# Performance work log

Hardware: AMD Instinct MI355X
Metric: run time of the kernel (lower is better)

The kernel has to match this reference:

```python
import jax, jax.numpy as jnp
import numpy as np

NUM_HEADS = 6
EPS = 1e-6

def setup_inputs() -> dict:
    key = jax.random.key(0)
    k1, k2, k3, k4, k5 = jax.random.split(key, 5)
    B, N, C = 8, 1024, 384
    x = jax.random.normal(k1, (B, N, C), dtype=jnp.float32)
    # torch nn.Linear weights stored here as [in, out] for y = x @ W
    w_qkv = jax.random.normal(k2, (C, 3 * C), dtype=jnp.float32) * 0.02
    w_out = jax.random.normal(k3, (C, C), dtype=jnp.float32) * 0.02
    b_out = jax.random.normal(k4, (C,), dtype=jnp.float32) * 0.02
    # non-negative random-walk visitation mask (avg visits per node)
    mask = jax.random.uniform(k5, (N, N), dtype=jnp.float32)
    return {"x": x, "w_qkv": w_qkv, "w_out": w_out, "b_out": b_out, "mask": mask}

def reference(x, w_qkv, w_out, b_out, mask):
    B, N, C = x.shape
    H = NUM_HEADS
    D = C // H
    qkv = x @ w_qkv                                   # [B,N,3C]
    q, k, v = jnp.split(qkv, 3, axis=-1)
    # [B,N,C] -> [B,H,N,D]
    to_heads = lambda t: t.reshape(B, N, H, D).transpose(0, 2, 1, 3)
    q, k, v = to_heads(q), to_heads(k), to_heads(v)
    # feature map: relu(x) + eps
    q = jax.nn.relu(q) + EPS
    k = jax.nn.relu(k) + EPS
    # masked linear kernel: (Phi(Q) Phi(K)^T * mask)
    kernel = jnp.einsum("bhnd,bhmd->bhnm", q, k) * mask  # [B,H,N,N]
    z = 1.0 / (kernel.sum(axis=-1, keepdims=True) + EPS)  # row normalizer
    out = jnp.einsum("bhnm,bhmd->bhnd", kernel, v) * z    # [B,H,N,D]
    out = out.transpose(0, 2, 1, 3).reshape(B, N, C)
    return out @ w_out + b_out
```

## Files before the change

kernel.cpp:

```cpp
#include <hip/hip_runtime.h>
#include <hip/hip_bf16.h>
#include <hip/hip_fp16.h>
#include <stdint.h>

typedef __hip_bfloat16 bf16;
typedef __attribute__((ext_vector_type(8))) short short8;
typedef __attribute__((ext_vector_type(4))) float f32x4;
typedef __attribute__((ext_vector_type(16))) float f32x16;
typedef __attribute__((ext_vector_type(4))) int int4v;
typedef __attribute__((ext_vector_type(4))) unsigned short ushort4v;

#define MFMA16(A,B,C) __builtin_amdgcn_mfma_f32_16x16x32_bf16(A,B,C,0,0,0)
#define MFMA32(A,B,C) __builtin_amdgcn_mfma_f32_32x32x16_bf16(A,B,C,0,0,0)

#define FENCE() asm volatile("" ::: "memory")
#define SBAR()  do { FENCE(); __builtin_amdgcn_s_barrier(); FENCE(); } while (0)
#define WAITVN(N) asm volatile("s_waitcnt vmcnt(" #N ")" ::: "memory")

static __device__ __forceinline__ void g2lds16(const void* g, void* l) {
  __builtin_amdgcn_global_load_lds(
      (__attribute__((address_space(1))) void*)(g),
      (__attribute__((address_space(3))) void*)(l), 16, 0, 0);
}

static __device__ __forceinline__ int swz8(int row, int kc) {
  return row * 8 + (kc ^ (row & 7));
}

static __device__ __forceinline__ unsigned short f2bf_bits(float f) {
  bf16 t = __float2bfloat16(f); unsigned short u; __builtin_memcpy(&u, &t, 2); return u;
}
static __device__ __forceinline__ unsigned short f2h_bits(float f) {
  __half t = __float2half(f); unsigned short u; __builtin_memcpy(&u, &t, 2); return u;
}

template<bool HALFOUT>
static __device__ __forceinline__ void tileT(const float* __restrict__ in,
                                             unsigned short* __restrict__ out,
                                             int R, int C, int tr, int tc, int tid,
                                             float (*tls)[65]) {
  const int rr0 = tid >> 4, c4 = tid & 15;
  #pragma unroll
  for (int rr = 0; rr < 4; ++rr) {
    int r = rr0 + rr * 16;
    float4 v = *(const float4*)(in + (size_t)(tr * 64 + r) * C + tc * 64 + c4 * 4);
    tls[r][c4 * 4 + 0] = v.x; tls[r][c4 * 4 + 1] = v.y;
    tls[r][c4 * 4 + 2] = v.z; tls[r][c4 * 4 + 3] = v.w;
  }
  __syncthreads();
  #pragma unroll
  for (int rr = 0; rr < 4; ++rr) {
    int r2 = rr0 + rr * 16;
    ushort4v o;
    #pragma unroll
    for (int k = 0; k < 4; ++k) {
      float f = tls[c4 * 4 + k][r2];
      o[k] = HALFOUT ? f2h_bits(f) : f2bf_bits(f);
    }
    *(ushort4v*)(out + (size_t)(tc * 64 + r2) * R + tr * 64 + c4 * 4) = o;
  }
}

__global__ __launch_bounds__(256)
void k_prep(const float* __restrict__ x, bf16* __restrict__ xb,
            const float* __restrict__ wqkv, unsigned short* __restrict__ wqkvT,
            const float* __restrict__ wout, unsigned short* __restrict__ woutT,
            const float* __restrict__ mask, unsigned short* __restrict__ maskT) {
  __shared__ float tls[64][65];
  const int bid = blockIdx.x, tid = threadIdx.x;
  if (bid < 768) {
    #pragma unroll
    for (int j = 0; j < 4; ++j) {
      int i = bid * 1024 + j * 256 + tid;
      float4 v = ((const float4*)x)[i];
      bf16* po = xb + (size_t)i * 4;
      po[0] = __float2bfloat16(v.x); po[1] = __float2bfloat16(v.y);
      po[2] = __float2bfloat16(v.z); po[3] = __float2bfloat16(v.w);
    }
  } else if (bid < 876) {
    int tt = bid - 768; tileT<false>(wqkv, wqkvT, 384, 1152, tt / 18, tt % 18, tid, tls);
  } else if (bid < 912) {
    int tt = bid - 876; tileT<false>(wout, woutT, 384, 384, tt / 6, tt % 6, tid, tls);
  } else {
    int tt = bid - 912; tileT<true>(mask, maskT, 1024, 1024, tt / 16, tt % 16, tid, tls);
  }
}

__global__ __launch_bounds__(256, 3)
void k_gemm_qkv(const bf16* __restrict__ A, const bf16* __restrict__ BT,
                bf16* __restrict__ Cb, bf16* __restrict__ vT)
{
  __shared__ __align__(16) bf16 As[128 * 64];
  __shared__ __align__(16) bf16 Bs[96 * 64];
  const int tid = threadIdx.x;
  const int wave = tid >> 6, lane = tid & 63;
  const int lhi = lane >> 4, llo = lane & 15;
  const int wr = wave >> 1, wc = wave & 1;
  const int mBase = blockIdx.x * 128, nBase = blockIdx.y * 96;
  const int K = 384, N = 1152;

  f32x4 acc[4][3] = {};

  for (int kt = 0; kt < K; kt += 64) {
    __syncthreads();
    #pragma unroll
    for (int i = 0; i < 4; ++i) {
      int c = i * 256 + tid;
      int row = c >> 3;
      int kc = (c & 7) ^ (row & 7);
      g2lds16(A + (size_t)(mBase + row) * K + kt + kc * 8, As + (c & ~63) * 8);
    }
    #pragma unroll
    for (int i = 0; i < 3; ++i) {
      int c = i * 256 + tid;
      int row = c >> 3;
      int kc = (c & 7) ^ (row & 7);
      g2lds16(BT + (size_t)(nBase + row) * K + kt + kc * 8, Bs + (c & ~63) * 8);
    }
    __syncthreads();
    for (int kk = 0; kk < 2; ++kk) {
      const int kc = kk * 4 + lhi;
      short8 a[4], b[3];
      #pragma unroll
      for (int mi = 0; mi < 4; ++mi)
        a[mi] = *(const short8*)(As + swz8(wr * 64 + mi * 16 + llo, kc) * 8);
      #pragma unroll
      for (int ni = 0; ni < 3; ++ni)
        b[ni] = *(const short8*)(Bs + swz8(wc * 48 + ni * 16 + llo, kc) * 8);
      #pragma unroll
      for (int mi = 0; mi < 4; ++mi)
        #pragma unroll
        for (int ni = 0; ni < 3; ++ni)
          acc[mi][ni] = MFMA16(a[mi], b[ni], acc[mi][ni]);
    }
  }

  const bool isV = (nBase >= 768);
  #pragma unroll
  for (int mi = 0; mi < 4; ++mi)
    #pragma unroll
    for (int ni = 0; ni < 3; ++ni) {
      const int colbase = nBase + wc * 48 + ni * 16;
      if (!isV) {
        #pragma unroll
        for (int j = 0; j < 4; ++j) {
          int row = mBase + wr * 64 + mi * 16 + lhi * 4 + j;
          int col = colbase + llo;
          float v = fmaxf(acc[mi][ni][j], 0.f) + 1e-6f;
          Cb[(size_t)row * N + col] = __float2bfloat16(v);
        }
      } else {
        int col = colbase + llo;
        int dall = col - 768, hh = dall >> 6, dd = dall & 63;
        int rowg = mBase + wr * 64 + mi * 16 + lhi * 4;
        int bb = rowg >> 10, nloc = rowg & 1023;
        ushort4v pk;
        #pragma unroll
        for (int j = 0; j < 4; ++j) pk[j] = f2bf_bits(acc[mi][ni][j]);
        *(ushort4v*)((unsigned short*)vT + (((size_t)bb * 6 + hh) * 64 + dd) * 1024 + nloc) = pk;
      }
    }
}

__global__ __launch_bounds__(256, 3)
void k_attn(const bf16* __restrict__ qkv,
            const bf16* __restrict__ vT,
            const __half* __restrict__ maskT,
            bf16* __restrict__ out)
{
  __shared__ __align__(16) bf16 Ks[2][64 * 64];
  __shared__ __align__(16) bf16 Vs[2][64 * 64];
  __shared__ float Ored[2][32][65];
  __shared__ float zred[2][2][32];

  const int bid = blockIdx.x;
  const int bh = bid % 48, qt = bid / 48;
  const int b = bh / 6, h = bh - b * 6;
  const int tid = threadIdx.x, wave = tid >> 6, lane = tid & 63;
  const int lq = lane & 31, lh = lane >> 5;
  const int wq = wave & 1, wm = wave >> 1;
  const size_t row0 = (size_t)b * 1024;
  const int qglob = qt * 64 + wq * 32 + lq;

  auto stageKV = [&](int mt, int buf) {
    #pragma unroll
    for (int i = 0; i < 2; ++i) {
      int c = (wave * 2 + i) * 64 + lane;
      int row = c >> 3;
      int kc = (c & 7) ^ (row & 7);
      g2lds16(qkv + (row0 + mt * 64 + row) * 1152 + 384 + h * 64 + kc * 8,
              Ks[buf] + (c & ~63) * 8);
      g2lds16(vT + ((size_t)bh * 64 + row) * 1024 + mt * 64 + kc * 8,
              Vs[buf] + (c & ~63) * 8);
    }
  };

  short8 bq[4];
  {
    const bf16* qp = qkv + (row0 + qglob) * 1152 + h * 64 + lh * 8;
    #pragma unroll
    for (int ks = 0; ks < 4; ++ks) bq[ks] = *(const short8*)(qp + ks * 16);
  }
  stageKV(0, 0);

  f32x16 accO[2] = {};
  float zl = 0.f;

  #pragma unroll 1
  for (int mt = 0; mt < 16; ++mt) {
    const int cur = mt & 1;
    const bf16* Kc = Ks[cur];
    const bf16* Vc = Vs[cur];

    if (mt < 15) {
      stageKV(mt + 1, cur ^ 1);
      WAITVN(4);
    } else {
      WAITVN(0);
    }
    SBAR();

    __half mv[16];
    {
      const int mrow0 = mt * 64 + wm * 32 + 4 * lh;
      #pragma unroll
      for (int g = 0; g < 4; ++g)
        #pragma unroll
        for (int j = 0; j < 4; ++j)
          mv[g * 4 + j] = maskT[(size_t)(mrow0 + 8 * g + j) * 1024 + qglob];
    }

    f32x16 st = {};
    #pragma unroll
    for (int ks = 0; ks < 4; ++ks) {
      int row = wm * 32 + lq;
      int cc = (ks * 2 + lh) ^ (row & 7);
      short8 af = *(const short8*)(Kc + (row * 8 + cc) * 8);
      st = MFMA32(af, bq[ks], st);
    }

    float p[16];
    {
      float zp = 0.f;
      #pragma unroll
      for (int r = 0; r < 16; ++r) {
        p[r] = st[r] * __half2float(mv[r]);
        zp += p[r];
      }
      zl += zp;
    }
    int u[4][2];
    #pragma unroll
    for (int g = 0; g < 4; ++g)
      #pragma unroll
      for (int c = 0; c < 2; ++c)
        asm("v_cvt_pk_bf16_f32 %0, %1, %2"
            : "=v"(u[g][c]) : "v"(p[4 * g + 2 * c]), "v"(p[4 * g + 2 * c + 1]));

    short8 pa[2];
    #pragma unroll
    for (int ks = 0; ks < 2; ++ks) {
      int A0 = u[2 * ks][0], A0b = u[2 * ks][1];
      int A1 = u[2 * ks + 1][0], A1b = u[2 * ks + 1][1];
      int x0 = __shfl_xor(A0, 32), x1 = __shfl_xor(A0b, 32);
      int y0 = __shfl_xor(A1, 32), y1 = __shfl_xor(A1b, 32);
      int4v iv;
      iv.x = lh ? y0 : A0;
      iv.y = lh ? y1 : A0b;
      iv.z = lh ? A1 : x0;
      iv.w = lh ? A1b : x1;
      pa[ks] = *(short8*)&iv;
    }

    #pragma unroll
    for (int db = 0; db < 2; ++db)
      #pragma unroll
      for (int ks = 0; ks < 2; ++ks) {
        int row = db * 32 + lq;
        int cc = (wm * 4 + ks * 2 + lh) ^ (row & 7);
        short8 vb = *(const short8*)(Vc + (row * 8 + cc) * 8);
        accO[db] = MFMA32(pa[ks], vb, accO[db]);
      }

    asm volatile("s_waitcnt lgkmcnt(0)" ::: "memory");
    __builtin_amdgcn_sched_barrier(0);
    SBAR();
  }

  zl += __shfl_xor(zl, 32);
  zred[wq][wm][lq] = zl;
  if (wm == 1) {
    #pragma unroll
    for (int db = 0; db < 2; ++db)
      #pragma unroll
      for (int r = 0; r < 16; ++r) {
        int q = (r & 3) + 8 * (r >> 2) + 4 * lh;
        Ored[wq][q][db * 32 + lq] = accO[db][r];
      }
  }
  __syncthreads();
  if (wm == 0) {
    #pragma unroll
    for (int r = 0; r < 16; ++r) {
      int q = (r & 3) + 8 * (r >> 2) + 4 * lh;
      float zt = zred[wq][0][q] + zred[wq][1][q];
      float zi = 1.f / (zt + 1e-6f);
      int n = qt * 64 + wq * 32 + q;
      size_t orow = (row0 + n) * 384 + h * 64;
      #pragma unroll
      for (int db = 0; db < 2; ++db) {
        float val = (accO[db][r] + Ored[wq][q][db * 32 + lq]) * zi;
        out[orow + db * 32 + lq] = __float2bfloat16(val);
      }
    }
  }
}

__global__ __launch_bounds__(256, 3)
void k_gemm_out(const bf16* __restrict__ A, const bf16* __restrict__ BT,
                float* __restrict__ Cf, const float* __restrict__ bias)
{
  __shared__ __align__(16) bf16 As[64 * 64];
  __shared__ __align__(16) bf16 Bs[64 * 64];
  const int tid = threadIdx.x;
  const int wave = tid >> 6, lane = tid & 63;
  const int lq = lane & 31, lh = lane >> 5;
  const int wr = wave >> 1, wc = wave & 1;
  const int mBase = blockIdx.x * 64, nBase = blockIdx.y * 64;
  const int N = 384, K = 384;

  f32x16 acc = {};
  for (int kt = 0; kt < K; kt += 64) {
    __syncthreads();
    #pragma unroll
    for (int i = 0; i < 2; ++i) {
      int c = (wave * 2 + i) * 64 + lane;
      int row = c >> 3;
      int kc = (c & 7) ^ (row & 7);
      g2lds16(A  + (size_t)(mBase + row) * K + kt + kc * 8, As + (c & ~63) * 8);
      g2lds16(BT + (size_t)(nBase + row) * K + kt + kc * 8, Bs + (c & ~63) * 8);
    }
    __syncthreads();
    #pragma unroll
    for (int ks = 0; ks < 4; ++ks) {
      int ra = wr * 32 + lq, rb = wc * 32 + lq;
      short8 a = *(const short8*)(As + (ra * 8 + ((ks * 2 + lh) ^ (ra & 7))) * 8);
      short8 b = *(const short8*)(Bs + (rb * 8 + ((ks * 2 + lh) ^ (rb & 7))) * 8);
      acc = MFMA32(a, b, acc);
    }
  }
  #pragma unroll
  for (int r = 0; r < 16; ++r) {
    int row = mBase + wr * 32 + (r & 3) + 8 * (r >> 2) + 4 * lh;
    int col = nBase + wc * 32 + lq;
    Cf[(size_t)row * N + col] = acc[r] + bias[col];
  }
}

extern "C" void kernel_launch(void* const* d_in, const int* in_sizes, int n_in,
                              void* d_out, int out_size, void* d_ws, size_t ws_size,
                              hipStream_t stream) {
  (void)in_sizes; (void)n_in; (void)out_size; (void)ws_size;
  const float* x    = (const float*)d_in[0];
  const float* wqkv = (const float*)d_in[1];
  const float* wout = (const float*)d_in[2];
  const float* bout = (const float*)d_in[3];
  const float* mask = (const float*)d_in[4];
  float* outp = (float*)d_out;

  char* ws = (char*)d_ws;
  bf16*  xb    = (bf16*)(ws);
  bf16*  wqkvT = (bf16*)(ws + 6291456);
  bf16*  woutT = (bf16*)(ws + 7176192);
  bf16*  qkvb  = (bf16*)(ws + 7471104);
  bf16*  vTb   = (bf16*)(ws + 26345472);
  bf16*  ab    = (bf16*)(ws + 32636928);
  __half* maskT = (__half*)(ws + 38928384);

  k_prep<<<dim3(1168), dim3(256), 0, stream>>>(
      x, xb, wqkv, (unsigned short*)wqkvT, wout, (unsigned short*)woutT,
      mask, (unsigned short*)maskT);

  k_gemm_qkv<<<dim3(64, 12), dim3(256), 0, stream>>>(xb, wqkvT, qkvb, vTb);
  k_attn<<<dim3(768), dim3(256), 0, stream>>>(qkvb, vTb, maskT, ab);
  k_gemm_out<<<dim3(128, 6), dim3(256), 0, stream>>>(ab, woutT, outp, bout);
}
```

Before: 58.81 us.

## Triple-buffer K/V tiles, prefetch mask one tile ahead, drop second barrier

The attention kernel now keeps K/V tiles in a three-slot ring inside one shared buffer, which lets each iteration get by with a single barrier instead of two. The per-tile mask values are loaded one iteration early into alternating register arrays, so global mask latency overlaps with the current tile's MFMA work. The Ored/zred reduction scratch now aliases the K/V staging memory, so total LDS stays at about 48.5KB. In exchange, register pressure rises from the extra mask array, and the ring-buffer reuse depends on barrier ordering being correct.

```diff
diff --git a/kernel.cpp b/kernel.cpp
--- a/kernel.cpp
+++ b/kernel.cpp
@@ -168,10 +168,11 @@
             const __half* __restrict__ maskT,
             bf16* __restrict__ out)
 {
-  __shared__ __align__(16) bf16 Ks[2][64 * 64];
-  __shared__ __align__(16) bf16 Vs[2][64 * 64];
-  __shared__ float Ored[2][32][65];
-  __shared__ float zred[2][2][32];
+  __shared__ __align__(16) char smem[49664];
+  bf16* KsB = (bf16*)smem;
+  bf16* VsB = KsB + 3 * 4096;
+  float* OredF = (float*)smem;
+  float* zredF = (float*)(smem + 49152);
 
   const int bid = blockIdx.x;
   const int bh = bid % 48, qt = bid / 48;
@@ -189,10 +190,18 @@
       int row = c >> 3;
       int kc = (c & 7) ^ (row & 7);
       g2lds16(qkv + (row0 + mt * 64 + row) * 1152 + 384 + h * 64 + kc * 8,
-              Ks[buf] + (c & ~63) * 8);
+              KsB + buf * 4096 + (c & ~63) * 8);
       g2lds16(vT + ((size_t)bh * 64 + row) * 1024 + mt * 64 + kc * 8,
-              Vs[buf] + (c & ~63) * 8);
-    }
+              VsB + buf * 4096 + (c & ~63) * 8);
+    }
+  };
+  auto loadMask = [&](int mt, __half (&mv)[16]) {
+    const int mrow0 = mt * 64 + wm * 32 + 4 * lh;
+    #pragma unroll
+    for (int g = 0; g < 4; ++g)
+      #pragma unroll
+      for (int j = 0; j < 4; ++j)
+        mv[g * 4 + j] = maskT[(size_t)(mrow0 + 8 * g + j) * 1024 + qglob];
   };
 
   short8 bq[4];
@@ -201,34 +210,29 @@
     #pragma unroll
     for (int ks = 0; ks < 4; ++ks) bq[ks] = *(const short8*)(qp + ks * 16);
   }
-  stageKV(0, 0);
 
   f32x16 accO[2] = {};
   float zl = 0.f;
 
-  #pragma unroll 1
-  for (int mt = 0; mt < 16; ++mt) {
-    const int cur = mt & 1;
-    const bf16* Kc = Ks[cur];
-    const bf16* Vc = Vs[cur];
-
-    if (mt < 15) {
-      stageKV(mt + 1, cur ^ 1);
+  __half mvA[16], mvB[16];
+  stageKV(0, 0);
+  loadMask(0, mvA);
+
+  auto iter = [&](int t, __half (&mvUse)[16], __half (&mvPre)[16]) {
+    const int bc = t % 3;
+    const bf16* Kc = KsB + bc * 4096;
+    const bf16* Vc = VsB + bc * 4096;
+
+    if (t < 15) {
+      stageKV(t + 1, (t + 1) % 3);
       WAITVN(4);
     } else {
       WAITVN(0);
     }
+    asm volatile("s_waitcnt lgkmcnt(0)" ::: "memory");
     SBAR();
 
-    __half mv[16];
-    {
-      const int mrow0 = mt * 64 + wm * 32 + 4 * lh;
-      #pragma unroll
-      for (int g = 0; g < 4; ++g)
-        #pragma unroll
-        for (int j = 0; j < 4; ++j)
-          mv[g * 4 + j] = maskT[(size_t)(mrow0 + 8 * g + j) * 1024 + qglob];
-    }
+    if (t < 15) loadMask(t + 1, mvPre);
 
     f32x16 st = {};
     #pragma unroll
@@ -244,7 +248,7 @@
       float zp = 0.f;
       #pragma unroll
       for (int r = 0; r < 16; ++r) {
-        p[r] = st[r] * __half2float(mv[r]);
+        p[r] = st[r] * __half2float(mvUse[r]);
         zp += p[r];
       }
       zl += zp;
@@ -281,21 +285,24 @@
         short8 vb = *(const short8*)(Vc + (row * 8 + cc) * 8);
         accO[db] = MFMA32(pa[ks], vb, accO[db]);
       }
-
-    asm volatile("s_waitcnt lgkmcnt(0)" ::: "memory");
-    __builtin_amdgcn_sched_barrier(0);
-    SBAR();
-  }
+  };
+
+  #pragma unroll 1
+  for (int mt2 = 0; mt2 < 8; ++mt2) {
+    iter(2 * mt2,     mvA, mvB);
+    iter(2 * mt2 + 1, mvB, mvA);
+  }
+  __syncthreads();
 
   zl += __shfl_xor(zl, 32);
-  zred[wq][wm][lq] = zl;
+  zredF[(wq * 2 + wm) * 32 + lq] = zl;
   if (wm == 1) {
     #pragma unroll
     for (int db = 0; db < 2; ++db)
       #pragma unroll
       for (int r = 0; r < 16; ++r) {
         int q = (r & 3) + 8 * (r >> 2) + 4 * lh;
-        Ored[wq][q][db * 32 + lq] = accO[db][r];
+        OredF[(wq * 32 + q) * 65 + db * 32 + lq] = accO[db][r];
       }
   }
   __syncthreads();
@@ -303,13 +310,13 @@
     #pragma unroll
     for (int r = 0; r < 16; ++r) {
       int q = (r & 3) + 8 * (r >> 2) + 4 * lh;
-      float zt = zred[wq][0][q] + zred[wq][1][q];
+      float zt = zredF[wq * 2 * 32 + q] + zredF[(wq * 2 + 1) * 32 + q];
       float zi = 1.f / (zt + 1e-6f);
       int n = qt * 64 + wq * 32 + q;
       size_t orow = (row0 + n) * 384 + h * 64;
       #pragma unroll
       for (int db = 0; db < 2; ++db) {
-        float val = (accO[db][r] + Ored[wq][q][db * 32 + lq]) * zi;
+        float val = (accO[db][r] + OredF[(wq * 32 + q) * 65 + db * 32 + lq]) * zi;
         out[orow + db * 32 + lq] = __float2bfloat16(val);
       }
     }
```

Measured after the change: 57.03 us. -3.0%, faster.

## Load K/V fragments directly from global memory instead of LDS double buffering

Applied to the files above, without the earlier changes.

The attention kernel drops its double-buffered LDS staging of K and V tiles (async global-to-LDS loads, waits and barriers). Each wave now reads its MFMA operands directly from global memory, relying on L1/L2 caching, and the loop is unrolled by two. This removes the barrier and LDS traffic cost and frees LDS, which may raise occupancy. In exchange, K/V data is fetched redundantly across waves, and global load latency is exposed without explicit prefetch.

```diff
diff --git a/kernel.cpp b/kernel.cpp
--- a/kernel.cpp
+++ b/kernel.cpp
@@ -12,10 +12,6 @@
 
 #define MFMA16(A,B,C) __builtin_amdgcn_mfma_f32_16x16x32_bf16(A,B,C,0,0,0)
 #define MFMA32(A,B,C) __builtin_amdgcn_mfma_f32_32x32x16_bf16(A,B,C,0,0,0)
-
-#define FENCE() asm volatile("" ::: "memory")
-#define SBAR()  do { FENCE(); __builtin_amdgcn_s_barrier(); FENCE(); } while (0)
-#define WAITVN(N) asm volatile("s_waitcnt vmcnt(" #N ")" ::: "memory")
 
 static __device__ __forceinline__ void g2lds16(const void* g, void* l) {
   __builtin_amdgcn_global_load_lds(
@@ -168,10 +164,8 @@
             const __half* __restrict__ maskT,
             bf16* __restrict__ out)
 {
-  __shared__ __align__(16) bf16 Ks[2][64 * 64];
-  __shared__ __align__(16) bf16 Vs[2][64 * 64];
-  __shared__ float Ored[2][32][65];
-  __shared__ float zred[2][2][32];
+  __shared__ float OredF[2][32][65];
+  __shared__ float zredF[2][2][32];
 
   const int bid = blockIdx.x;
   const int bh = bid % 48, qt = bid / 48;
@@ -182,60 +176,33 @@
   const size_t row0 = (size_t)b * 1024;
   const int qglob = qt * 64 + wq * 32 + lq;
 
-  auto stageKV = [&](int mt, int buf) {
-    #pragma unroll
-    for (int i = 0; i < 2; ++i) {
-      int c = (wave * 2 + i) * 64 + lane;
-      int row = c >> 3;
-      int kc = (c & 7) ^ (row & 7);
-      g2lds16(qkv + (row0 + mt * 64 + row) * 1152 + 384 + h * 64 + kc * 8,
-              Ks[buf] + (c & ~63) * 8);
-      g2lds16(vT + ((size_t)bh * 64 + row) * 1024 + mt * 64 + kc * 8,
-              Vs[buf] + (c & ~63) * 8);
-    }
-  };
-
   short8 bq[4];
   {
     const bf16* qp = qkv + (row0 + qglob) * 1152 + h * 64 + lh * 8;
     #pragma unroll
     for (int ks = 0; ks < 4; ++ks) bq[ks] = *(const short8*)(qp + ks * 16);
   }
-  stageKV(0, 0);
+
+  const bf16* kpl = qkv + (row0 + wm * 32 + lq) * 1152 + 384 + h * 64 + lh * 8;
+  const bf16* vpl = vT + ((size_t)bh * 64 + lq) * 1024 + wm * 32 + lh * 8;
+  const __half* mpl = maskT + (size_t)(wm * 32 + 4 * lh) * 1024 + qglob;
 
   f32x16 accO[2] = {};
   float zl = 0.f;
 
-  #pragma unroll 1
+  #pragma unroll 2
   for (int mt = 0; mt < 16; ++mt) {
-    const int cur = mt & 1;
-    const bf16* Kc = Ks[cur];
-    const bf16* Vc = Vs[cur];
-
-    if (mt < 15) {
-      stageKV(mt + 1, cur ^ 1);
-      WAITVN(4);
-    } else {
-      WAITVN(0);
-    }
-    SBAR();
-
     __half mv[16];
-    {
-      const int mrow0 = mt * 64 + wm * 32 + 4 * lh;
-      #pragma unroll
-      for (int g = 0; g < 4; ++g)
-        #pragma unroll
-        for (int j = 0; j < 4; ++j)
-          mv[g * 4 + j] = maskT[(size_t)(mrow0 + 8 * g + j) * 1024 + qglob];
-    }
+    #pragma unroll
+    for (int g = 0; g < 4; ++g)
+      #pragma unroll
+      for (int j = 0; j < 4; ++j)
+        mv[g * 4 + j] = mpl[(size_t)(mt * 64 + 8 * g + j) * 1024];
 
     f32x16 st = {};
     #pragma unroll
     for (int ks = 0; ks < 4; ++ks) {
-      int row = wm * 32 + lq;
-      int cc = (ks * 2 + lh) ^ (row & 7);
-      short8 af = *(const short8*)(Kc + (row * 8 + cc) * 8);
+      short8 af = *(const short8*)(kpl + (size_t)mt * 64 * 1152 + ks * 16);
       st = MFMA32(af, bq[ks], st);
     }
 
@@ -276,26 +243,20 @@
     for (int db = 0; db < 2; ++db)
       #pragma unroll
       for (int ks = 0; ks < 2; ++ks) {
-        int row = db * 32 + lq;
-        int cc = (wm * 4 + ks * 2 + lh) ^ (row & 7);
-        short8 vb = *(const short8*)(Vc + (row * 8 + cc) * 8);
+        short8 vb = *(const short8*)(vpl + (size_t)db * 32 * 1024 + mt * 64 + ks * 16);
         accO[db] = MFMA32(pa[ks], vb, accO[db]);
       }
-
-    asm volatile("s_waitcnt lgkmcnt(0)" ::: "memory");
-    __builtin_amdgcn_sched_barrier(0);
-    SBAR();
   }
 
   zl += __shfl_xor(zl, 32);
-  zred[wq][wm][lq] = zl;
+  zredF[wq][wm][lq] = zl;
   if (wm == 1) {
     #pragma unroll
     for (int db = 0; db < 2; ++db)
       #pragma unroll
       for (int r = 0; r < 16; ++r) {
         int q = (r & 3) + 8 * (r >> 2) + 4 * lh;
-        Ored[wq][q][db * 32 + lq] = accO[db][r];
+        OredF[wq][q][db * 32 + lq] = accO[db][r];
       }
   }
   __syncthreads();
@@ -303,13 +264,13 @@
     #pragma unroll
     for (int r = 0; r < 16; ++r) {
       int q = (r & 3) + 8 * (r >> 2) + 4 * lh;
-      float zt = zred[wq][0][q] + zred[wq][1][q];
+      float zt = zredF[wq][0][q] + zredF[wq][1][q];
       float zi = 1.f / (zt + 1e-6f);
       int n = qt * 64 + wq * 32 + q;
       size_t orow = (row0 + n) * 384 + h * 64;
       #pragma unroll
       for (int db = 0; db < 2; ++db) {
-        float val = (accO[db][r] + Ored[wq][q][db * 32 + lq]) * zi;
+        float val = (accO[db][r] + OredF[wq][q][db * 32 + lq]) * zi;
         out[orow + db * 32 + lq] = __float2bfloat16(val);
       }
     }
```

Result: slower. 92.31 us (+56.9%).
